# Kernel tuning notes

Measured on AMD Instinct MI355X. Metric: run time of the kernel, lower is better.

## Reference

```python
import jax, jax.numpy as jnp
import numpy as np

B, S, IN_DIM, OUT_DIM, G = 8, 2048, 512, 256, 8
CHUNK = 128  # positions per scan step; per-chunk phi = CHUNK*O*O*G floats
EPS = 1e-5   # torch LayerNorm default


def make_periods():
    # periods[i,j,g] = i*(O*G) + j*G + g + 2
    i = jnp.arange(OUT_DIM, dtype=jnp.float32)[:, None, None]
    j = jnp.arange(OUT_DIM, dtype=jnp.float32)[None, :, None]
    g = jnp.arange(G, dtype=jnp.float32)[None, None, :]
    return i * (OUT_DIM * G) + j * G + g + 2.0


def setup_inputs() -> dict:
    key = jax.random.key(0)
    ks = jax.random.split(key, 4)
    x = jax.random.normal(ks[0], (B, S, IN_DIM), dtype=jnp.float32)
    positions = jnp.arange(S, dtype=jnp.int64 if jax.config.jax_enable_x64 else jnp.int32)
    M = jax.random.uniform(ks[1], (OUT_DIM, IN_DIM), minval=-0.5, maxval=0.5, dtype=jnp.float32)
    P = jax.random.uniform(ks[2], (OUT_DIM, OUT_DIM, G), minval=-0.1, maxval=0.1, dtype=jnp.float32)
    W_res = jax.random.uniform(ks[3], (OUT_DIM, IN_DIM), minval=-0.1, maxval=0.1, dtype=jnp.float32)
    ln_scale = jnp.ones((OUT_DIM,), dtype=jnp.float32)
    ln_bias = jnp.zeros((OUT_DIM,), dtype=jnp.float32)
    periods = make_periods()
    return {"x": x, "M": M, "P": P, "W_res": W_res, "ln_scale": ln_scale,
            "ln_bias": ln_bias, "periods": periods, "positions": positions}


def layer_norm(h, scale, bias):
    mu = jnp.mean(h, axis=-1, keepdims=True)
    var = jnp.mean(jnp.square(h - mu), axis=-1, keepdims=True)  # biased, like torch
    return (h - mu) * jax.lax.rsqrt(var + EPS) * scale + bias


def reference(x, M, P, W_res, ln_scale, ln_bias, periods, positions):
    # x: (B,S,in), M: (out,in), P: (out,out,G), periods: (out,out,G)
    x_trans = layer_norm(jnp.einsum('bsi,oi->bso', x, M), ln_scale, ln_bias)

    two_pi = jnp.float32(2.0 * np.pi)
    pos_chunks = positions.astype(jnp.float32).reshape(-1, CHUNK)  # (S/CHUNK, CHUNK)

    def body(carry, pos):
        # phi: (CHUNK, O, O, G); reduce over g first to avoid the huge 5D tensor
        phi = jnp.cos(two_pi * pos[:, None, None, None] / periods)
        A = jnp.einsum('sijg,ijg->sij', phi, P)  # (CHUNK, O, O)
        return carry, A

    _, A = jax.lax.scan(body, 0, pos_chunks)
    A = A.reshape(S, OUT_DIM, OUT_DIM)  # A[s,i,j] = sum_g P[i,j,g]*cos(2*pi*k_s/T_ijg)

    Nk = jnp.einsum('bsj,sij->bsi', x_trans, A)  # (B,S,out)
    residual = jnp.einsum('bsi,oi->bso', x, W_res)  # separate residual proj
    return Nk + residual
```

## Files before the change

### kernel.cpp

```cpp
#include <hip/hip_runtime.h>
#include <hip/hip_bf16.h>
#include <math.h>

#define B_   8
#define S_   2048
#define IN_  512
#define OUT_ 256
#define G_   8


typedef float  f32x2  __attribute__((ext_vector_type(2)));
typedef float  f32x4  __attribute__((ext_vector_type(4)));
typedef short  s16x8  __attribute__((ext_vector_type(8)));
typedef __bf16 bf16x8 __attribute__((ext_vector_type(8)));
typedef unsigned short u16x8 __attribute__((ext_vector_type(8)));

__device__ __forceinline__ float cos2pi(float f) {
#if __has_builtin(__builtin_amdgcn_cosf)
    return __builtin_amdgcn_cosf(f);
#else
    return __cosf(6.28318530717958647692f * f);
#endif
}

__device__ __forceinline__ float fractf_(float f) {
#if __has_builtin(__builtin_amdgcn_fractf)
    return __builtin_amdgcn_fractf(f);
#else
    return f - floorf(f);
#endif
}

__device__ __forceinline__ unsigned short f2bf(float f) {
    unsigned u = __builtin_bit_cast(unsigned, f);
    u += 0x7fffu + ((u >> 16) & 1u);
    return (unsigned short)(u >> 16);
}

template <typename T>
__device__ __forceinline__ auto atomF_(T* p, T v, int) -> decltype(unsafeAtomicAdd(p, v)) {
    return unsafeAtomicAdd(p, v);
}
template <typename T>
__device__ __forceinline__ T atomF_(T* p, T v, long) {
    return atomicAdd(p, v);
}
__device__ __forceinline__ void atomAddF(float* p, float v) { atomF_(p, v, 0); }

template <typename T>
__device__ __forceinline__ auto mfma_bf16_(T a, T b, f32x4 c, int)
    -> decltype(__builtin_amdgcn_mfma_f32_16x16x32_bf16(a, b, c, 0, 0, 0)) {
    return __builtin_amdgcn_mfma_f32_16x16x32_bf16(a, b, c, 0, 0, 0);
}
template <typename T>
__device__ __forceinline__ auto mfma_bf16_(T a, T b, f32x4 c, long)
    -> decltype(__builtin_amdgcn_mfma_f32_16x16x32_bf16(__builtin_bit_cast(bf16x8, a),
                                                        __builtin_bit_cast(bf16x8, b), c, 0, 0, 0)) {
    return __builtin_amdgcn_mfma_f32_16x16x32_bf16(__builtin_bit_cast(bf16x8, a),
                                                   __builtin_bit_cast(bf16x8, b), c, 0, 0, 0);
}
__device__ __forceinline__ f32x4 mfma_bf16(s16x8 a, s16x8 b, f32x4 c) {
    return mfma_bf16_(a, b, c, 0);
}

__device__ __forceinline__ void gld16(const void* g, void* l) {
    __builtin_amdgcn_global_load_lds((const __attribute__((address_space(1))) unsigned int*)g,
                                     (__attribute__((address_space(3))) unsigned int*)l,
                                     16, 0, 0);
}

__device__ __forceinline__ f32x2 lo2(float4 v) { f32x2 r; r.x = v.x; r.y = v.y; return r; }
__device__ __forceinline__ f32x2 hi2(float4 v) { f32x2 r; r.x = v.z; r.y = v.w; return r; }

__device__ __forceinline__ void prep_one(const float* __restrict__ P,
                                         const float* __restrict__ periods,
                                         float4* __restrict__ PTK, int tid) {
    const int j = tid >> 8, i = tid & 255;
    float p[8], iT[8], k2[8];
#pragma unroll
    for (int g = 0; g < 8; ++g) {
        const int idx = (i * 256 + j) * 8 + g;
        p[g]  = P[idx];
        iT[g] = 1.0f / periods[idx];
        k2[g] = 2.0f * cos2pi(iT[g]);
    }
    float4* base = PTK + (size_t)(j * 6) * 256 + i;
    base[0]    = make_float4(p[0],  p[1],  p[2],  p[3]);
    base[256]  = make_float4(p[4],  p[5],  p[6],  p[7]);
    base[512]  = make_float4(iT[0], iT[1], iT[2], iT[3]);
    base[768]  = make_float4(iT[4], iT[5], iT[6], iT[7]);
    base[1024] = make_float4(k2[0], k2[1], k2[2], k2[3]);
    base[1280] = make_float4(k2[4], k2[5], k2[6], k2[7]);
}

__global__ __launch_bounds__(256) void cvt_prep(const float* __restrict__ x,
                                                const float* __restrict__ M,
                                                const float* __restrict__ Wres,
                                                const float* __restrict__ P,
                                                const float* __restrict__ periods,
                                                unsigned short* __restrict__ Xb,
                                                unsigned short* __restrict__ Wb,
                                                float4* __restrict__ PTK) {
    const int bid = blockIdx.x;
    if (bid >= 4224) {
        prep_one(P, periods, PTK, (bid - 4224) * 256 + threadIdx.x);
        return;
    }
    const float* src;
    unsigned short* dst;
    if (bid < 4096) {
        const int idx = bid * 256 + threadIdx.x;
        src = x + (size_t)idx * 8;
        dst = Xb + (size_t)idx * 8;
    } else {
        const int idx = (bid - 4096) * 256 + threadIdx.x;
        const int row = idx >> 6;
        const int col = (idx & 63) * 8;
        src = (row < 256) ? (M + (size_t)row * 512 + col)
                          : (Wres + (size_t)(row - 256) * 512 + col);
        dst = Wb + (size_t)row * 512 + col;
    }
    const float4 v0 = *(const float4*)(src);
    const float4 v1 = *(const float4*)(src + 4);
    u16x8 o;
    o[0] = f2bf(v0.x); o[1] = f2bf(v0.y); o[2] = f2bf(v0.z); o[3] = f2bf(v0.w);
    o[4] = f2bf(v1.x); o[5] = f2bf(v1.y); o[6] = f2bf(v1.z); o[7] = f2bf(v1.w);
    *(u16x8*)dst = o;
}

__global__ __launch_bounds__(256) void cvt_xw(const float* __restrict__ x,
                                              const float* __restrict__ M,
                                              const float* __restrict__ Wres,
                                              unsigned short* __restrict__ Xb,
                                              unsigned short* __restrict__ Wb) {
    const int bid = blockIdx.x;
    const float* src;
    unsigned short* dst;
    if (bid < 4096) {
        const int idx = bid * 256 + threadIdx.x;
        src = x + (size_t)idx * 8;
        dst = Xb + (size_t)idx * 8;
    } else {
        const int idx = (bid - 4096) * 256 + threadIdx.x;
        const int row = idx >> 6;
        const int col = (idx & 63) * 8;
        src = (row < 256) ? (M + (size_t)row * 512 + col)
                          : (Wres + (size_t)(row - 256) * 512 + col);
        dst = Wb + (size_t)row * 512 + col;
    }
    const float4 v0 = *(const float4*)(src);
    const float4 v1 = *(const float4*)(src + 4);
    u16x8 o;
    o[0] = f2bf(v0.x); o[1] = f2bf(v0.y); o[2] = f2bf(v0.z); o[3] = f2bf(v0.w);
    o[4] = f2bf(v1.x); o[5] = f2bf(v1.y); o[6] = f2bf(v1.z); o[7] = f2bf(v1.w);
    *(u16x8*)dst = o;
}

__global__ __launch_bounds__(256) void prep_ptk(const float* __restrict__ P,
                                                const float* __restrict__ periods,
                                                float4* __restrict__ PTK) {
    prep_one(P, periods, PTK, blockIdx.x * 256 + threadIdx.x);
}

__global__ __launch_bounds__(256) void gemm_mfma(const unsigned short* __restrict__ Xb,
                                                 const unsigned short* __restrict__ Wb,
                                                 float* __restrict__ y,
                                                 float* __restrict__ out) {
    __shared__ __align__(16) unsigned short At[64 * 64];
    __shared__ __align__(16) unsigned short Bt[128 * 64];
    const int t    = threadIdx.x;
    const int col0 = blockIdx.x * 128;
    const int row0 = blockIdx.y * 64;

    const unsigned short* ga[2]; int la[2];
    const unsigned short* gb[4]; int lb[4];
#pragma unroll
    for (int cc = 0; cc < 2; ++cc) {
        const int L = cc * 256 + t;
        const int r = L >> 3;
        const int c = (L & 7) ^ (r & 7);
        ga[cc] = Xb + (size_t)(row0 + r) * 512 + c * 8;
        la[cc] = L * 8;
    }
#pragma unroll
    for (int cc = 0; cc < 4; ++cc) {
        const int L = cc * 256 + t;
        const int r = L >> 3;
        const int c = (L & 7) ^ (r & 7);
        gb[cc] = Wb + (size_t)(col0 + r) * 512 + c * 8;
        lb[cc] = L * 8;
    }

    const int lane = t & 63;
    const int wave = t >> 6;
    const int wn   = wave * 32;
    const int quad = lane >> 4;
    const int l16  = lane & 15;

    f32x4 acc[4][2];
#pragma unroll
    for (int mi = 0; mi < 4; ++mi)
#pragma unroll
        for (int ni = 0; ni < 2; ++ni) acc[mi][ni] = {0.0f, 0.0f, 0.0f, 0.0f};

    for (int k0 = 0; k0 < 512; k0 += 64) {
        __syncthreads();
#pragma unroll
        for (int cc = 0; cc < 2; ++cc) gld16(ga[cc] + k0, At + la[cc]);
#pragma unroll
        for (int cc = 0; cc < 4; ++cc) gld16(gb[cc] + k0, Bt + lb[cc]);
        __syncthreads();
#pragma unroll
        for (int ks = 0; ks < 2; ++ks) {
            const int cc = (ks * 4 + quad) ^ (l16 & 7);
            s16x8 af[4], bf[2];
#pragma unroll
            for (int mi = 0; mi < 4; ++mi) {
                const int ra = mi * 16 + l16;
                af[mi] = *(const s16x8*)(At + (ra * 8 + cc) * 8);
            }
#pragma unroll
            for (int ni = 0; ni < 2; ++ni) {
                const int rb = wn + ni * 16 + l16;
                bf[ni] = *(const s16x8*)(Bt + (rb * 8 + cc) * 8);
            }
#pragma unroll
            for (int mi = 0; mi < 4; ++mi)
#pragma unroll
                for (int ni = 0; ni < 2; ++ni)
                    acc[mi][ni] = mfma_bf16(af[mi], bf[ni], acc[mi][ni]);
        }
    }

    float* dst   = (col0 < 256) ? y : out;
    const int cb = (col0 & 255) + wn;
#pragma unroll
    for (int mi = 0; mi < 4; ++mi) {
        const int rbase = row0 + mi * 16 + quad * 4;
#pragma unroll
        for (int ni = 0; ni < 2; ++ni) {
            const int col = cb + ni * 16 + l16;
#pragma unroll
            for (int rg = 0; rg < 4; ++rg)
                dst[(size_t)(rbase + rg) * 256 + col] = acc[mi][ni][rg];
        }
    }
}

__global__ __launch_bounds__(256) void gemm_kernel(const float* __restrict__ x,
                                                   const float* __restrict__ M,
                                                   const float* __restrict__ Wres,
                                                   float* __restrict__ y,
                                                   float* __restrict__ out) {
    __shared__ float As[8][132];
    __shared__ float Bs[8][132];
    const int ct = blockIdx.x;
    const int rt = blockIdx.y;
    const int t  = threadIdx.x;
    const int row0 = rt * 128;
    const float* W = (ct < 2) ? M : Wres;
    const int wcol0 = (ct & 1) * 128;
    float acc[8][8];
#pragma unroll
    for (int r = 0; r < 8; ++r)
#pragma unroll
        for (int c = 0; c < 8; ++c) acc[r][c] = 0.0f;
    const int lr = t >> 1;
    const int lk = (t & 1) << 2;
    for (int k0 = 0; k0 < 512; k0 += 8) {
        float4 av = *(const float4*)(x + (size_t)(row0 + lr) * 512 + k0 + lk);
        float4 bv = *(const float4*)(W + (size_t)(wcol0 + lr) * 512 + k0 + lk);
        __syncthreads();
        As[lk + 0][lr] = av.x; As[lk + 1][lr] = av.y; As[lk + 2][lr] = av.z; As[lk + 3][lr] = av.w;
        Bs[lk + 0][lr] = bv.x; Bs[lk + 1][lr] = bv.y; Bs[lk + 2][lr] = bv.z; Bs[lk + 3][lr] = bv.w;
        __syncthreads();
        const int tx = t & 15, ty = t >> 4;
#pragma unroll
        for (int kk = 0; kk < 8; ++kk) {
            const float4 a0 = *(const float4*)&As[kk][ty * 8];
            const float4 a1 = *(const float4*)&As[kk][ty * 8 + 4];
            const float4 b0 = *(const float4*)&Bs[kk][tx * 8];
            const float4 b1 = *(const float4*)&Bs[kk][tx * 8 + 4];
            const float ar[8] = {a0.x, a0.y, a0.z, a0.w, a1.x, a1.y, a1.z, a1.w};
            const float br[8] = {b0.x, b0.y, b0.z, b0.w, b1.x, b1.y, b1.z, b1.w};
#pragma unroll
            for (int r = 0; r < 8; ++r)
#pragma unroll
                for (int c = 0; c < 8; ++c) acc[r][c] = fmaf(ar[r], br[c], acc[r][c]);
        }
    }
    const int tx = t & 15, ty = t >> 4;
    float* dst = (ct < 2) ? y : out;
    const int cbase = (ct & 1) * 128 + tx * 8;
#pragma unroll
    for (int r = 0; r < 8; ++r) {
        float4 v0 = {acc[r][0], acc[r][1], acc[r][2], acc[r][3]};
        float4 v1 = {acc[r][4], acc[r][5], acc[r][6], acc[r][7]};
        float* p = dst + (size_t)(row0 + ty * 8 + r) * 256 + cbase;
        *(float4*)(p)     = v0;
        *(float4*)(p + 4) = v1;
    }
}

__global__ __launch_bounds__(256) void ln_kernel(float* __restrict__ y,
                                                 const float* __restrict__ scale,
                                                 const float* __restrict__ bias) {
    const int t    = threadIdx.x;
    const int row  = blockIdx.x * 4 + (t >> 6);
    const int lane = t & 63;
    float* p = y + (size_t)row * 256 + lane * 4;
    float4 v = *(float4*)p;
    float s  = v.x + v.y + v.z + v.w;
    float ss = v.x * v.x + v.y * v.y + v.z * v.z + v.w * v.w;
#pragma unroll
    for (int off = 32; off > 0; off >>= 1) {
        s  += __shfl_xor(s, off);
        ss += __shfl_xor(ss, off);
    }
    const float mu  = s * (1.0f / 256.0f);
    const float var = ss * (1.0f / 256.0f) - mu * mu;
    const float rs  = rsqrtf(var + 1e-5f);
    float4 sc = *(const float4*)(scale + lane * 4);
    float4 bi = *(const float4*)(bias + lane * 4);
    float4 o;
    o.x = (v.x - mu) * rs * sc.x + bi.x;
    o.y = (v.y - mu) * rs * sc.y + bi.y;
    o.z = (v.z - mu) * rs * sc.z + bi.z;
    o.w = (v.w - mu) * rs * sc.w + bi.w;
    *(float4*)p = o;
}

__global__ __launch_bounds__(256, 4) void cosnk_pk(const float4* __restrict__ PTK,
                                                   const float* __restrict__ xt,
                                                   float* __restrict__ out) {
    __shared__ float xs[128 * 64];
    const int t  = threadIdx.x;
    const int bx = blockIdx.x;
    const int ih = (bx >> 2) & 1;
    const int rid = ((bx >> 3) << 2) | (bx & 3);
    const int stile = rid >> 1;
    const int jh = rid & 1;
    const int s0 = stile * 8;
    const int jbase = jh * 128;

    {
        const int slot = t >> 2;
        const int st   = slot >> 3;
        const int b    = slot & 7;
        const int jg   = t & 3;
        const float* src = xt + (size_t)(b * S_ + s0 + st) * 256 + jbase + jg * 32;
#pragma unroll
        for (int q = 0; q < 8; ++q) {
            float4 v = *(const float4*)(src + 4 * q);
            const int jl = jg * 32 + 4 * q;
            xs[(jl + 0) * 64 + slot] = v.x;
            xs[(jl + 1) * 64 + slot] = v.y;
            xs[(jl + 2) * 64 + slot] = v.z;
            xs[(jl + 3) * 64 + slot] = v.w;
        }
    }
    __syncthreads();

    const int i   = ih * 128 + (t & 127);
    const int jq  = t >> 7;
    const int jl0 = jq * 64;
    const float sv0 = (float)s0;
    f32x2 sv0v; sv0v.x = sv0; sv0v.y = sv0;

    f32x2 accP[8][4];
#pragma unroll
    for (int s = 0; s < 8; ++s)
#pragma unroll
        for (int q = 0; q < 4; ++q) { accP[s][q].x = 0.0f; accP[s][q].y = 0.0f; }

    const float4* ptk = PTK + (size_t)(jbase + jl0) * 1536 + i;
    float4 qp0 = ptk[0],    qp1 = ptk[256];
    float4 qt0 = ptk[512],  qt1 = ptk[768];
    float4 qk0 = ptk[1024], qk1 = ptk[1280];

#define CHEBP(p2_, t2_, k2_)                                \
    do {                                                    \
        f32x2 f0 = sv0v * (t2_);                            \
        f0.x = fractf_(f0.x); f0.y = fractf_(f0.y);         \
        f32x2 c0; c0.x = cos2pi(f0.x); c0.y = cos2pi(f0.y); \
        f32x2 f1 = f0 + (t2_);                              \
        f1.x = fractf_(f1.x); f1.y = fractf_(f1.y);         \
        f32x2 c1; c1.x = cos2pi(f1.x); c1.y = cos2pi(f1.y); \
        f32x2 c2 = (k2_) * c1 - c0;                         \
        f32x2 c3 = (k2_) * c2 - c1;                         \
        f32x2 c4 = (k2_) * c3 - c2;                         \
        f32x2 c5 = (k2_) * c4 - c3;                         \
        f32x2 c6 = (k2_) * c5 - c4;                         \
        f32x2 c7 = (k2_) * c6 - c5;                         \
        A0 += (p2_) * c0; A1 += (p2_) * c1;                 \
        A2 += (p2_) * c2; A3 += (p2_) * c3;                 \
        A4 += (p2_) * c4; A5 += (p2_) * c5;                 \
        A6 += (p2_) * c6; A7 += (p2_) * c7;                 \
    } while (0)

    for (int jj = 0; jj < 64; ++jj) {
        const float4* pn = ptk + ((jj < 63) ? 1536 : 0);
        const float4 n0 = pn[0],   n1 = pn[256],  n2 = pn[512];
        const float4 n3 = pn[768], n4 = pn[1024], n5 = pn[1280];

        f32x2 A0 = {0.f, 0.f}, A1 = {0.f, 0.f}, A2 = {0.f, 0.f}, A3 = {0.f, 0.f};
        f32x2 A4 = {0.f, 0.f}, A5 = {0.f, 0.f}, A6 = {0.f, 0.f}, A7 = {0.f, 0.f};
        CHEBP(lo2(qp0), lo2(qt0), lo2(qk0));
        CHEBP(hi2(qp0), hi2(qt0), hi2(qk0));
        CHEBP(lo2(qp1), lo2(qt1), lo2(qk1));
        CHEBP(hi2(qp1), hi2(qt1), hi2(qk1));

        const float as_[8] = {A0.x + A0.y, A1.x + A1.y, A2.x + A2.y, A3.x + A3.y,
                              A4.x + A4.y, A5.x + A5.y, A6.x + A6.y, A7.x + A7.y};

        const float* xrow = &xs[(jl0 + jj) * 64];
#pragma unroll
        for (int s = 0; s < 8; ++s) {
            const float4 xa = *(const float4*)(xrow + s * 8);
            const float4 xb = *(const float4*)(xrow + s * 8 + 4);
            f32x2 av; av.x = as_[s]; av.y = as_[s];
            accP[s][0] += av * lo2(xa);
            accP[s][1] += av * hi2(xa);
            accP[s][2] += av * lo2(xb);
            accP[s][3] += av * hi2(xb);
        }
        qp0 = n0; qp1 = n1; qt0 = n2; qt1 = n3; qk0 = n4; qk1 = n5;
        ptk = pn;
    }
#undef CHEBP

    __syncthreads();
    const int tl = t & 127;
    if (jq) {
#pragma unroll
        for (int slot = 0; slot < 64; ++slot) {
            const int st = slot >> 3, b = slot & 7;
            xs[slot * 128 + tl] = accP[st][b >> 1][b & 1];
        }
    }
    __syncthreads();
    if (!jq) {
#pragma unroll
        for (int slot = 0; slot < 64; ++slot) {
            const int st = slot >> 3, b = slot & 7;
            const float v = accP[st][b >> 1][b & 1] + xs[slot * 128 + tl];
            atomAddF(&out[(size_t)(b * S_ + s0 + st) * 256 + i], v);
        }
    }
}

extern "C" void kernel_launch(void* const* d_in, const int* in_sizes, int n_in,
                              void* d_out, int out_size, void* d_ws, size_t ws_size,
                              hipStream_t stream) {
    const float* x        = (const float*)d_in[0];
    const float* M        = (const float*)d_in[1];
    const float* P        = (const float*)d_in[2];
    const float* Wres     = (const float*)d_in[3];
    const float* ln_scale = (const float*)d_in[4];
    const float* ln_bias  = (const float*)d_in[5];
    const float* periods  = (const float*)d_in[6];

    float* out = (float*)d_out;
    char*  wsb = (char*)d_ws;
    const size_t MB = 1024 * 1024;
    float* y = (float*)wsb;
    unsigned short* Xb = (unsigned short*)(wsb + 16 * MB);
    unsigned short* Wb = (unsigned short*)(wsb + 32 * MB);

    const bool big  = (ws_size >= 39 * MB);
    const bool mfma = (ws_size >= (size_t)34078720);

    float4* PTK;
    if (big) {
        PTK = (float4*)(wsb + 33 * MB);
        cvt_prep<<<4480, 256, 0, stream>>>(x, M, Wres, P, periods, Xb, Wb, PTK);
        dim3 ggrid(4, 256);
        gemm_mfma<<<ggrid, 256, 0, stream>>>(Xb, Wb, y, out);
    } else if (mfma) {
        PTK = (float4*)(wsb + 16 * MB);
        cvt_xw<<<4224, 256, 0, stream>>>(x, M, Wres, Xb, Wb);
        dim3 ggrid(4, 256);
        gemm_mfma<<<ggrid, 256, 0, stream>>>(Xb, Wb, y, out);
        prep_ptk<<<256, 256, 0, stream>>>(P, periods, PTK);
    } else {
        PTK = (float4*)(wsb + 16 * MB);
        dim3 ggrid(4, 128);
        gemm_kernel<<<ggrid, 256, 0, stream>>>(x, M, Wres, y, out);
        prep_ptk<<<256, 256, 0, stream>>>(P, periods, PTK);
    }

    ln_kernel<<<4096, 256, 0, stream>>>(y, ln_scale, ln_bias);

    cosnk_pk<<<1024, 256, 0, stream>>>(PTK, y, out);
}
```

Before: 236.4 us.

## Write LayerNorm output in tile-transposed layout and read it directly in cosnk

Adds a LayerNorm kernel that writes normalized activations into a layout grouped by 8-position tile, column and batch. Adds a cosnk variant that reads x rows straight from global memory in that layout instead of staging them through shared memory. Both are used on the large-workspace path. This removes the LDS staging load phase and its barrier, at the cost of scattered strided stores in LayerNorm and per-iteration global loads that depend on cache hits.

```diff
diff --git a/kernel.cpp b/kernel.cpp
--- a/kernel.cpp
+++ b/kernel.cpp
@@ -330,6 +330,42 @@
     *(float4*)p = o;
 }
 
+__global__ __launch_bounds__(256) void ln_t(const float* __restrict__ y,
+                                            const float* __restrict__ scale,
+                                            const float* __restrict__ bias,
+                                            float* __restrict__ xt2) {
+    const int t    = threadIdx.x;
+    const int row  = blockIdx.x * 4 + (t >> 6);
+    const int lane = t & 63;
+    const float* p = y + (size_t)row * 256 + lane * 4;
+    float4 v = *(const float4*)p;
+    float s  = v.x + v.y + v.z + v.w;
+    float ss = v.x * v.x + v.y * v.y + v.z * v.z + v.w * v.w;
+#pragma unroll
+    for (int off = 32; off > 0; off >>= 1) {
+        s  += __shfl_xor(s, off);
+        ss += __shfl_xor(ss, off);
+    }
+    const float mu  = s * (1.0f / 256.0f);
+    const float var = ss * (1.0f / 256.0f) - mu * mu;
+    const float rs  = rsqrtf(var + 1e-5f);
+    float4 sc = *(const float4*)(scale + lane * 4);
+    float4 bi = *(const float4*)(bias + lane * 4);
+    float4 o;
+    o.x = (v.x - mu) * rs * sc.x + bi.x;
+    o.y = (v.y - mu) * rs * sc.y + bi.y;
+    o.z = (v.z - mu) * rs * sc.z + bi.z;
+    o.w = (v.w - mu) * rs * sc.w + bi.w;
+    const int b = row >> 11;
+    const int sidx = row & 2047;
+    float* dst = xt2 + (size_t)(sidx >> 3) * 16384 + (size_t)lane * 256
+                     + (sidx & 7) * 8 + b;
+    dst[0]   = o.x;
+    dst[64]  = o.y;
+    dst[128] = o.z;
+    dst[192] = o.w;
+}
+
 __global__ __launch_bounds__(256, 4) void cosnk_pk(const float4* __restrict__ PTK,
                                                    const float* __restrict__ xt,
                                                    float* __restrict__ out) {
@@ -427,6 +463,89 @@
         qp0 = n0; qp1 = n1; qt0 = n2; qt1 = n3; qk0 = n4; qk1 = n5;
         ptk = pn;
     }
+
+    __syncthreads();
+    const int tl = t & 127;
+    if (jq) {
+#pragma unroll
+        for (int slot = 0; slot < 64; ++slot) {
+            const int st = slot >> 3, b = slot & 7;
+            xs[slot * 128 + tl] = accP[st][b >> 1][b & 1];
+        }
+    }
+    __syncthreads();
+    if (!jq) {
+#pragma unroll
+        for (int slot = 0; slot < 64; ++slot) {
+            const int st = slot >> 3, b = slot & 7;
+            const float v = accP[st][b >> 1][b & 1] + xs[slot * 128 + tl];
+            atomAddF(&out[(size_t)(b * S_ + s0 + st) * 256 + i], v);
+        }
+    }
+}
+
+__global__ __launch_bounds__(256, 4) void cosnk_sx(const float4* __restrict__ PTK,
+                                                   const float* __restrict__ xt2,
+                                                   float* __restrict__ out) {
+    __shared__ float xs[64 * 128];
+    const int t  = threadIdx.x;
+    const int bx = blockIdx.x;
+    const int ih = (bx >> 2) & 1;
+    const int rid = ((bx >> 3) << 2) | (bx & 3);
+    const int stile = rid >> 1;
+    const int jh = rid & 1;
+    const int s0 = stile * 8;
+    const int jbase = jh * 128;
+
+    const int i   = ih * 128 + (t & 127);
+    const int jq  = t >> 7;
+    const int jl0 = jq * 64;
+    const int jqu = __builtin_amdgcn_readfirstlane(jq);
+    const float* xcol = xt2 + (size_t)stile * 16384 + (size_t)(jbase + jqu * 64) * 64;
+
+    const float sv0 = (float)s0;
+    f32x2 sv0v; sv0v.x = sv0; sv0v.y = sv0;
+
+    f32x2 accP[8][4];
+#pragma unroll
+    for (int s = 0; s < 8; ++s)
+#pragma unroll
+        for (int q = 0; q < 4; ++q) { accP[s][q].x = 0.0f; accP[s][q].y = 0.0f; }
+
+    const float4* ptk = PTK + (size_t)(jbase + jl0) * 1536 + i;
+    float4 qp0 = ptk[0],    qp1 = ptk[256];
+    float4 qt0 = ptk[512],  qt1 = ptk[768];
+    float4 qk0 = ptk[1024], qk1 = ptk[1280];
+
+    for (int jj = 0; jj < 64; ++jj) {
+        const float* xrow = xcol + jj * 64;
+        const float4* pn = ptk + ((jj < 63) ? 1536 : 0);
+        const float4 n0 = pn[0],   n1 = pn[256],  n2 = pn[512];
+        const float4 n3 = pn[768], n4 = pn[1024], n5 = pn[1280];
+
+        f32x2 A0 = {0.f, 0.f}, A1 = {0.f, 0.f}, A2 = {0.f, 0.f}, A3 = {0.f, 0.f};
+        f32x2 A4 = {0.f, 0.f}, A5 = {0.f, 0.f}, A6 = {0.f, 0.f}, A7 = {0.f, 0.f};
+        CHEBP(lo2(qp0), lo2(qt0), lo2(qk0));
+        CHEBP(hi2(qp0), hi2(qt0), hi2(qk0));
+        CHEBP(lo2(qp1), lo2(qt1), lo2(qk1));
+        CHEBP(hi2(qp1), hi2(qt1), hi2(qk1));
+
+        const float as_[8] = {A0.x + A0.y, A1.x + A1.y, A2.x + A2.y, A3.x + A3.y,
+                              A4.x + A4.y, A5.x + A5.y, A6.x + A6.y, A7.x + A7.y};
+
+#pragma unroll
+        for (int s = 0; s < 8; ++s) {
+            const float4 xa = *(const float4*)(xrow + s * 8);
+            const float4 xb = *(const float4*)(xrow + s * 8 + 4);
+            f32x2 av; av.x = as_[s]; av.y = as_[s];
+            accP[s][0] += av * lo2(xa);
+            accP[s][1] += av * hi2(xa);
+            accP[s][2] += av * lo2(xb);
+            accP[s][3] += av * hi2(xb);
+        }
+        qp0 = n0; qp1 = n1; qt0 = n2; qt1 = n3; qk0 = n4; qk1 = n5;
+        ptk = pn;
+    }
 #undef CHEBP
 
     __syncthreads();
@@ -473,23 +592,26 @@
     float4* PTK;
     if (big) {
         PTK = (float4*)(wsb + 33 * MB);
+        float* xt2 = (float*)(wsb + 16 * MB);
         cvt_prep<<<4480, 256, 0, stream>>>(x, M, Wres, P, periods, Xb, Wb, PTK);
         dim3 ggrid(4, 256);
         gemm_mfma<<<ggrid, 256, 0, stream>>>(Xb, Wb, y, out);
+        ln_t<<<4096, 256, 0, stream>>>(y, ln_scale, ln_bias, xt2);
+        cosnk_sx<<<1024, 256, 0, stream>>>(PTK, xt2, out);
     } else if (mfma) {
         PTK = (float4*)(wsb + 16 * MB);
         cvt_xw<<<4224, 256, 0, stream>>>(x, M, Wres, Xb, Wb);
         dim3 ggrid(4, 256);
         gemm_mfma<<<ggrid, 256, 0, stream>>>(Xb, Wb, y, out);
         prep_ptk<<<256, 256, 0, stream>>>(P, periods, PTK);
+        ln_kernel<<<4096, 256, 0, stream>>>(y, ln_scale, ln_bias);
+        cosnk_pk<<<1024, 256, 0, stream>>>(PTK, y, out);
     } else {
         PTK = (float4*)(wsb + 16 * MB);
         dim3 ggrid(4, 128);
         gemm_kernel<<<ggrid, 256, 0, stream>>>(x, M, Wres, y, out);
         prep_ptk<<<256, 256, 0, stream>>>(P, periods, PTK);
-    }
-
-    ln_kernel<<<4096, 256, 0, stream>>>(y, ln_scale, ln_bias);
-
-    cosnk_pk<<<1024, 256, 0, stream>>>(PTK, y, out);
-}
+        ln_kernel<<<4096, 256, 0, stream>>>(y, ln_scale, ln_bias);
+        cosnk_pk<<<1024, 256, 0, stream>>>(PTK, y, out);
+    }
+}
```

Result: slower. 306.5 us (+29.6%).
